# Kernel tuning notes

Measured on AMD Instinct MI355X. Metric: run time of the kernel, lower is better.

Reference implementation:

```python
import jax, jax.numpy as jnp
import numpy as np

N_BLOCKS = 16
BLOCK_SIZE = 512
TOP_K = N_BLOCKS // 4  # matches n_blocks // 4 in the source


def setup_inputs() -> dict:
    key = jax.random.key(0)
    k1, k2, k3, k4, k5 = jax.random.split(key, 5)
    in_f, out_f = 2048, 8192
    x = jax.random.normal(k1, (2, 4096, in_f), dtype=jnp.float32)
    # router: Linear(in_features, n_blocks)
    Wr = jax.random.normal(k2, (N_BLOCKS, in_f), dtype=jnp.float32) * (in_f ** -0.5)
    br = jnp.zeros((N_BLOCKS,), dtype=jnp.float32)
    # fc1: Linear(in, out); fc2: Linear(out, in). Biases are unused in the original forward.
    W1 = jax.random.normal(k3, (out_f, in_f), dtype=jnp.float32) * (in_f ** -0.5)
    W2 = jax.random.normal(k4, (in_f, out_f), dtype=jnp.float32) * (out_f ** -0.5)
    return {"x": x, "Wr": Wr, "br": br, "W1": W1, "W2": W2}


def reference(x, Wr, br, W1, W2):
    x_shape = x.shape
    in_f = x_shape[-1]
    xf = x.reshape(-1, in_f)                      # [N, in]
    n = xf.shape[0]
    # router + top-k block selection per token
    prob = jax.nn.softmax(xf @ Wr.T + br, axis=-1)          # [N, nb]
    _, idx = jax.lax.top_k(prob, TOP_K)                      # [N, k]
    mask = jnp.zeros((n, N_BLOCKS), dtype=xf.dtype)
    mask = mask.at[jnp.arange(n)[:, None], idx].set(1.0)     # [N, nb]
    # fc1 per block: h[n,i,b] = x @ W1_block_i^T  (bias never used in source)
    W1b = W1.reshape(N_BLOCKS, BLOCK_SIZE, in_f)
    h = jnp.einsum('nf,ibf->nib', xf, W1b)                   # [N, nb, bs]
    # activation, then zero out unselected blocks (unselected never reach fc2)
    h = jax.nn.gelu(h, approximate=False) * mask[:, :, None]
    # fc2 per block accumulate: y = sum_i h_i @ W2_block_i^T
    W2b = W2.reshape(in_f, N_BLOCKS, BLOCK_SIZE)
    y = jnp.einsum('nib,fib->nf', h, W2b)                    # [N, in]
    return y.reshape(x_shape)
```

## Files before the change

kernel.cpp:

```cpp
#include <hip/hip_runtime.h>
#include <hip/hip_bf16.h>

#define N_TOK 8192
#define IN_F  2048
#define OUT_F 8192
#define NB    16
#define BS    512
#define BM2   256
#define MAX_MT2 144

typedef short          bf16x8  __attribute__((ext_vector_type(8)));
typedef unsigned short ushort8 __attribute__((ext_vector_type(8)));
typedef float          f32x4   __attribute__((ext_vector_type(4)));
typedef _Float16       f16x8   __attribute__((ext_vector_type(8)));

#define WS_COUNTS 0
#define WS_TSTART 64
#define WS_SEL    256
#define WS_INV    (32*1024)
#define WS_LISTS  (192*1024)
#define WS_XBF    (1ull<<20)
#define WS_W2BF   WS_XBF
#define WS_H      (WS_XBF + 33554432ull)
#define WS_W1BF   (WS_H + 37748736ull)
#define WS_YP     WS_W1BF

static __device__ __forceinline__ unsigned short f2bf(float f) {
    __hip_bfloat16 h = __float2bfloat16(f);
    return *reinterpret_cast<unsigned short*>(&h);
}

static __device__ __forceinline__ void gload16(const unsigned short* g, unsigned short* lds) {
    __builtin_amdgcn_global_load_lds(
        (const __attribute__((address_space(1))) unsigned int*)g,
        (__attribute__((address_space(3))) unsigned int*)lds, 16, 0, 0);
}

#define MFMA16(ai, bi) \
    acc[0][0] = __builtin_amdgcn_mfma_f32_16x16x32_bf16(ai##0, bi##0, acc[0][0], 0, 0, 0); \
    acc[0][1] = __builtin_amdgcn_mfma_f32_16x16x32_bf16(ai##0, bi##1, acc[0][1], 0, 0, 0); \
    acc[0][2] = __builtin_amdgcn_mfma_f32_16x16x32_bf16(ai##0, bi##2, acc[0][2], 0, 0, 0); \
    acc[0][3] = __builtin_amdgcn_mfma_f32_16x16x32_bf16(ai##0, bi##3, acc[0][3], 0, 0, 0); \
    acc[1][0] = __builtin_amdgcn_mfma_f32_16x16x32_bf16(ai##1, bi##0, acc[1][0], 0, 0, 0); \
    acc[1][1] = __builtin_amdgcn_mfma_f32_16x16x32_bf16(ai##1, bi##1, acc[1][1], 0, 0, 0); \
    acc[1][2] = __builtin_amdgcn_mfma_f32_16x16x32_bf16(ai##1, bi##2, acc[1][2], 0, 0, 0); \
    acc[1][3] = __builtin_amdgcn_mfma_f32_16x16x32_bf16(ai##1, bi##3, acc[1][3], 0, 0, 0); \
    acc[2][0] = __builtin_amdgcn_mfma_f32_16x16x32_bf16(ai##2, bi##0, acc[2][0], 0, 0, 0); \
    acc[2][1] = __builtin_amdgcn_mfma_f32_16x16x32_bf16(ai##2, bi##1, acc[2][1], 0, 0, 0); \
    acc[2][2] = __builtin_amdgcn_mfma_f32_16x16x32_bf16(ai##2, bi##2, acc[2][2], 0, 0, 0); \
    acc[2][3] = __builtin_amdgcn_mfma_f32_16x16x32_bf16(ai##2, bi##3, acc[2][3], 0, 0, 0); \
    acc[3][0] = __builtin_amdgcn_mfma_f32_16x16x32_bf16(ai##3, bi##0, acc[3][0], 0, 0, 0); \
    acc[3][1] = __builtin_amdgcn_mfma_f32_16x16x32_bf16(ai##3, bi##1, acc[3][1], 0, 0, 0); \
    acc[3][2] = __builtin_amdgcn_mfma_f32_16x16x32_bf16(ai##3, bi##2, acc[3][2], 0, 0, 0); \
    acc[3][3] = __builtin_amdgcn_mfma_f32_16x16x32_bf16(ai##3, bi##3, acc[3][3], 0, 0, 0);

#define PHASE_TAIL \
    __builtin_amdgcn_s_barrier(); \
    asm volatile("s_waitcnt lgkmcnt(0)" ::: "memory"); \
    __builtin_amdgcn_sched_barrier(0); \
    __builtin_amdgcn_s_setprio(1); \
    MFMA16(a, b) \
    __builtin_amdgcn_s_setprio(0); \
    __builtin_amdgcn_sched_barrier(0); \
    __builtin_amdgcn_s_barrier();

__global__ __launch_bounds__(256) void router_kernel(
    const float* __restrict__ x, const float* __restrict__ Wr,
    const float* __restrict__ br, unsigned short* __restrict__ sel,
    unsigned short* __restrict__ x_bf)
{
    __shared__ float xs[4][IN_F];
    const int tid = threadIdx.x;
    const int lt = tid & 63;
    const int wv = tid >> 6;
    const int tok = blockIdx.x * 4 + wv;
    float4* xl = (float4*)xs[wv];
    const float4* xp = (const float4*)(x + (size_t)tok * IN_F);
    #pragma unroll
    for (int i = 0; i < 8; ++i) xl[lt + i * 64] = xp[lt + i * 64];
    __syncthreads();
    const int e = lt >> 2, p = lt & 3;
    const float4* wp = (const float4*)(Wr + (size_t)e * IN_F);
    double s = 0.0;
    for (int j = p; j < IN_F / 4; j += 4) {
        float4 a = xl[j], w = wp[j];
        s += (double)a.x * w.x + (double)a.y * w.y + (double)a.z * w.z + (double)a.w * w.w;
    }
    s += __shfl_down(s, 2);
    s += __shfl_down(s, 1);
    __shared__ double logits[4][NB];
    if (p == 0) logits[wv][e] = s + (double)br[e];
    __syncthreads();
    if (lt == 0) {
        unsigned used = 0, packed = 0;
        #pragma unroll
        for (int kk = 0; kk < 4; ++kk) {
            int best = 0; double bv = -1.0e300;
            #pragma unroll
            for (int i = 0; i < NB; ++i)
                if (!((used >> i) & 1u) && logits[wv][i] > bv) { bv = logits[wv][i]; best = i; }
            used |= 1u << best;
            packed |= (unsigned)best << (4 * kk);
        }
        sel[tok] = (unsigned short)packed;
    }
    const int t7 = tok & 7;
    unsigned short* drow = x_bf + (size_t)tok * IN_F;
    #pragma unroll
    for (int i = 0; i < 4; ++i) {
        const int slot = lt + i * 64;
        const float* sp = &xs[wv][slot * 8];
        ushort8 o;
        #pragma unroll
        for (int j = 0; j < 8; ++j) o[j] = f2bf(sp[j]);
        *(ushort8*)(drow + ((slot ^ t7) << 3)) = o;
    }
}

__global__ __launch_bounds__(256) void build_lists_kernel(
    const unsigned short* __restrict__ sel, int* __restrict__ counts,
    int* __restrict__ lists, unsigned* __restrict__ inv)
{
    const int e = blockIdx.x;
    const int t = threadIdx.x;
    unsigned short mysel[N_TOK / 256];
    int cnt = 0;
    #pragma unroll
    for (int i = 0; i < N_TOK / 256; ++i) {
        unsigned s = sel[i * 256 + t];
        mysel[i] = (unsigned short)s;
        bool m = ((s & 15u) == (unsigned)e) | (((s >> 4) & 15u) == (unsigned)e) |
                 (((s >> 8) & 15u) == (unsigned)e) | (((s >> 12) & 15u) == (unsigned)e);
        cnt += m ? 1 : 0;
    }
    __shared__ int ps[256];
    ps[t] = cnt;
    __syncthreads();
    #pragma unroll
    for (int off = 1; off < 256; off <<= 1) {
        int v = (t >= off) ? ps[t - off] : 0;
        __syncthreads();
        ps[t] += v;
        __syncthreads();
    }
    int pos = ps[t] - cnt;
    if (t == 255) counts[e] = ps[255];
    #pragma unroll
    for (int i = 0; i < N_TOK / 256; ++i) {
        unsigned s = mysel[i];
        bool m = ((s & 15u) == (unsigned)e) | (((s >> 4) & 15u) == (unsigned)e) |
                 (((s >> 8) & 15u) == (unsigned)e) | (((s >> 12) & 15u) == (unsigned)e);
        if (m) {
            const int tok = i * 256 + t;
            int j = ((s & 15u) == (unsigned)e) ? 0 :
                    (((s >> 4) & 15u) == (unsigned)e) ? 1 :
                    (((s >> 8) & 15u) == (unsigned)e) ? 2 : 3;
            inv[tok * 4 + j] = ((unsigned)e << 16) | (unsigned)pos;
            lists[e * N_TOK + pos++] = tok;
        }
    }
}

__global__ void scan_kernel(const int* __restrict__ counts, int* __restrict__ tstart)
{
    if (threadIdx.x == 0) {
        int acc = 0;
        for (int i = 0; i < NB; ++i) { tstart[i] = acc; acc += (counts[i] + BM2 - 1) / BM2; }
        tstart[NB] = acc;
    }
}

__global__ __launch_bounds__(256) void convert_swz_kernel(
    const float* __restrict__ src, unsigned short* __restrict__ dst, int sh)
{
    const int total = 1 << 21;
    for (int id = blockIdx.x * 256 + threadIdx.x; id < total; id += 2048 * 256) {
        const int row = id >> sh;
        const int sr  = id & ((1 << sh) - 1);
        const int ps  = sr ^ (row & 7);
        const float4* s4 = (const float4*)(src + ((size_t)id << 3));
        float4 p0 = s4[0], p1 = s4[1];
        ushort8 o;
        o[0] = f2bf(p0.x); o[1] = f2bf(p0.y); o[2] = f2bf(p0.z); o[3] = f2bf(p0.w);
        o[4] = f2bf(p1.x); o[5] = f2bf(p1.y); o[6] = f2bf(p1.z); o[7] = f2bf(p1.w);
        *(ushort8*)(dst + (((size_t)(row) << sh) << 3) + ((size_t)ps << 3)) = o;
    }
}

__global__ __launch_bounds__(512) void fc1_kernel(
    const unsigned short* __restrict__ x_bf, const unsigned short* __restrict__ w1_bf,
    const int* __restrict__ lists, const int* __restrict__ counts,
    const int* __restrict__ tstart, unsigned short* __restrict__ h)
{
    __shared__ unsigned short lds[73728];
    const int bid = blockIdx.x;
    const int newid = (bid & 7) * 72 + (bid >> 3);
    const int nt = newid & 3, mt = newid >> 2;
    if (mt >= tstart[NB]) return;
    int b = 0;
    #pragma unroll
    for (int i = 1; i < NB; ++i) b += (mt >= tstart[i]);
    const int cnt  = counts[b];
    const int row0 = (mt - tstart[b]) * BM2;
    const int tid  = threadIdx.x;
    const int wave = tid >> 6, lane = tid & 63;
    const int sph = lane & 7;
    const int rbase = wave * 8 + (lane >> 3);

    const unsigned short* aS[4];
    const unsigned short* bS[2];
    #pragma unroll
    for (int i = 0; i < 4; ++i) {
        const int r = i * 64 + rbase;
        const int gr = min(row0 + r, cnt - 1);
        const int tok = lists[b * N_TOK + gr];
        aS[i] = x_bf + (size_t)tok * IN_F + ((sph ^ (r & 7) ^ (tok & 7)) << 3);
    }
    #pragma unroll
    for (int j = 0; j < 2; ++j) {
        const int r = j * 64 + rbase;
        bS[j] = w1_bf + (size_t)(b * BS + nt * 128 + r) * IN_F + (sph << 3);
    }
    const int wbase = wave * 512;

    const int lr16 = lane & 15, q = lane >> 4;
    const int wm = (wave >> 1) * 64, wn = (wave & 1) * 64;
    int offA[4], offB[4];
    #pragma unroll
    for (int i = 0; i < 4; ++i) { const int r = wm + i * 16 + lr16; offA[i] = r * 64 + ((q ^ (r & 7)) << 3); }
    #pragma unroll
    for (int j = 0; j < 4; ++j) { const int r = wn + j * 16 + lr16; offB[j] = r * 64 + ((q ^ (r & 7)) << 3); }

    f32x4 acc[4][4];
    #pragma unroll
    for (int i = 0; i < 4; ++i)
        #pragma unroll
        for (int j = 0; j < 4; ++j) acc[i][j] = (f32x4)0.0f;

#define STA1(k, buf, i) gload16(aS[i] + (size_t)(k) * 64, lds + (buf) * 24576 + (i) * 4096 + wbase)
#define STB1(k, buf, j) gload16(bS[j] + (size_t)(k) * 64, lds + (buf) * 24576 + 16384 + (j) * 4096 + wbase)

    STA1(0,0,0); STA1(0,0,1); STA1(0,0,2); STA1(0,0,3); STB1(0,0,0); STB1(0,0,1);
    STA1(1,1,0); STA1(1,1,1); STA1(1,1,2); STA1(1,1,3); STB1(1,1,0); STB1(1,1,1);
    asm volatile("s_waitcnt vmcnt(6)" ::: "memory");
    __builtin_amdgcn_s_barrier();

    const int NK = IN_F / 64;
    int cur = 0;
    for (int k = 0; k < NK; ++k) {
        const unsigned short* Ab = lds + cur * 24576;
        const unsigned short* Bb = Ab + 16384;
        const int nxt = (cur == 0) ? 2 : cur - 1;
        bf16x8 a0 = *(const bf16x8*)&Ab[offA[0]];
        bf16x8 a1 = *(const bf16x8*)&Ab[offA[1]];
        bf16x8 a2 = *(const bf16x8*)&Ab[offA[2]];
        bf16x8 a3 = *(const bf16x8*)&Ab[offA[3]];
        bf16x8 b0 = *(const bf16x8*)&Bb[offB[0]];
        bf16x8 b1 = *(const bf16x8*)&Bb[offB[1]];
        bf16x8 b2 = *(const bf16x8*)&Bb[offB[2]];
        bf16x8 b3 = *(const bf16x8*)&Bb[offB[3]];
        if (k + 2 < NK) { STA1(k + 2, nxt, 0); STA1(k + 2, nxt, 1); STB1(k + 2, nxt, 0); }
        PHASE_TAIL
        a0 = *(const bf16x8*)&Ab[offA[0] ^ 32];
        a1 = *(const bf16x8*)&Ab[offA[1] ^ 32];
        a2 = *(const bf16x8*)&Ab[offA[2] ^ 32];
        a3 = *(const bf16x8*)&Ab[offA[3] ^ 32];
        b0 = *(const bf16x8*)&Bb[offB[0] ^ 32];
        b1 = *(const bf16x8*)&Bb[offB[1] ^ 32];
        b2 = *(const bf16x8*)&Bb[offB[2] ^ 32];
        b3 = *(const bf16x8*)&Bb[offB[3] ^ 32];
        if (k + 2 < NK) {
            STA1(k + 2, nxt, 2); STA1(k + 2, nxt, 3); STB1(k + 2, nxt, 1);
            asm volatile("s_waitcnt vmcnt(6)" ::: "memory");
        } else if (k + 1 < NK) {
            asm volatile("s_waitcnt vmcnt(0)" ::: "memory");
        }
        PHASE_TAIL
        cur = (cur == 2) ? 0 : cur + 1;
    }
    #pragma unroll
    for (int i = 0; i < 4; ++i) {
        #pragma unroll
        for (int r = 0; r < 4; ++r) {
            const int lrow = wm + i * 16 + q * 4 + r;
            if (row0 + lrow < cnt) {
                const size_t hrow = (size_t)(mt * BM2 + lrow) * BS;
                const int r7 = (lrow & 7) << 3;
                #pragma unroll
                for (int j = 0; j < 4; ++j) {
                    const int col = nt * 128 + wn + j * 16 + lr16;
                    float v = acc[i][j][r];
                    v = 0.5f * v * (1.0f + erff(v * 0.70710678118654752f));
                    h[hrow + (col ^ r7)] = f2bf(v);
                }
            }
        }
    }
#undef STA1
#undef STB1
}

__global__ __launch_bounds__(512) void fc2_kernel(
    const unsigned short* __restrict__ h, const unsigned short* __restrict__ w2_bf,
    const int* __restrict__ counts, const int* __restrict__ tstart,
    _Float16* __restrict__ yp)
{
    __shared__ unsigned short lds[2][32768];
    const int bid = blockIdx.x;
    const int newid = (bid & 7) * 144 + (bid >> 3);
    const int nt = newid & 7, mt = newid >> 3;
    if (mt >= tstart[NB]) return;
    int b = 0;
    #pragma unroll
    for (int i = 1; i < NB; ++i) b += (mt >= tstart[i]);
    const int cnt  = counts[b];
    const int row0 = (mt - tstart[b]) * BM2;
    const int tid  = threadIdx.x;
    const int wave = tid >> 6, lane = tid & 63;
    const int sph = lane & 7;
    const int rbase = wave * 8 + (lane >> 3);

    const unsigned short* aS[4];
    const unsigned short* bS[4];
    #pragma unroll
    for (int g = 0; g < 4; ++g) {
        const int r = g * 64 + rbase;
        aS[g] = h + (size_t)(mt * BM2 + r) * BS + (sph << 3);
        bS[g] = w2_bf + (size_t)(nt * 256 + r) * OUT_F + b * BS + (sph << 3);
    }
    const int wbase = wave * 512;

    const int lr16 = lane & 15, q = lane >> 4;
    const int wr = (wave >> 2) * 128, wc = (wave & 3) * 64;
    int offA[8], offB[4];
    #pragma unroll
    for (int i = 0; i < 8; ++i) { const int r = wr + i * 16 + lr16; offA[i] = r * 64 + ((q ^ (r & 7)) << 3); }
    #pragma unroll
    for (int j = 0; j < 4; ++j) { const int r = wc + j * 16 + lr16; offB[j] = 16384 + r * 64 + ((q ^ (r & 7)) << 3); }

    f32x4 acc[8][4];
    #pragma unroll
    for (int i = 0; i < 8; ++i)
        #pragma unroll
        for (int j = 0; j < 4; ++j) acc[i][j] = (f32x4)0.0f;

#define ST2(k, buf) \
    { _Pragma("unroll") for (int g = 0; g < 4; ++g) \
        gload16(aS[g] + (size_t)(k) * 64, &lds[buf][g * 4096 + wbase]); \
      _Pragma("unroll") for (int g = 0; g < 4; ++g) \
        gload16(bS[g] + (size_t)(k) * 64, &lds[buf][16384 + g * 4096 + wbase]); }

#define MFMA_8x4 \
    __builtin_amdgcn_s_barrier(); \
    asm volatile("s_waitcnt lgkmcnt(0)" ::: "memory"); \
    __builtin_amdgcn_sched_barrier(0); \
    __builtin_amdgcn_s_setprio(1); \
    _Pragma("unroll") for (int i = 0; i < 8; ++i) \
        _Pragma("unroll") for (int j = 0; j < 4; ++j) \
            acc[i][j] = __builtin_amdgcn_mfma_f32_16x16x32_bf16(a[i], bb[j], acc[i][j], 0, 0, 0); \
    __builtin_amdgcn_s_setprio(0); \
    __builtin_amdgcn_sched_barrier(0); \
    __builtin_amdgcn_s_barrier();

    ST2(0, 0);
    asm volatile("s_waitcnt vmcnt(0)" ::: "memory");
    __builtin_amdgcn_s_barrier();

    const int NK = BS / 64;
    for (int k = 0; k < NK; ++k) {
        const int cur = k & 1;
        const unsigned short* L = lds[cur];
        {
            bf16x8 a[8], bb[4];
            #pragma unroll
            for (int i = 0; i < 8; ++i) a[i]  = *(const bf16x8*)&L[offA[i]];
            #pragma unroll
            for (int j = 0; j < 4; ++j) bb[j] = *(const bf16x8*)&L[offB[j]];
            if (k + 1 < NK) ST2(k + 1, cur ^ 1);
            MFMA_8x4
        }
        {
            bf16x8 a[8], bb[4];
            #pragma unroll
            for (int i = 0; i < 8; ++i) a[i]  = *(const bf16x8*)&L[offA[i] ^ 32];
            #pragma unroll
            for (int j = 0; j < 4; ++j) bb[j] = *(const bf16x8*)&L[offB[j] ^ 32];
            if (k + 1 < NK) asm volatile("s_waitcnt vmcnt(0)" ::: "memory");
            MFMA_8x4
        }
    }
    #pragma unroll
    for (int i = 0; i < 8; ++i) {
        #pragma unroll
        for (int r = 0; r < 4; ++r) {
            const int lrow = wr + i * 16 + q * 4 + r;
            if (row0 + lrow < cnt) {
                _Float16* yrow = yp + (size_t)(mt * BM2 + lrow) * IN_F + nt * 256 + wc + lr16;
                #pragma unroll
                for (int j = 0; j < 4; ++j)
                    yrow[j * 16] = (_Float16)acc[i][j][r];
            }
        }
    }
#undef ST2
#undef MFMA_8x4
}

__global__ __launch_bounds__(256) void reduce_kernel(
    const _Float16* __restrict__ yp, const unsigned* __restrict__ inv,
    const int* __restrict__ tstart, float* __restrict__ y)
{
    const int tok = blockIdx.x;
    __shared__ size_t rbase[4];
    if (threadIdx.x < 4) {
        unsigned v = inv[tok * 4 + threadIdx.x];
        rbase[threadIdx.x] = (size_t)(tstart[v >> 16] * BM2 + (int)(v & 0xFFFFu)) * IN_F;
    }
    __syncthreads();
    const int c = threadIdx.x * 8;
    f16x8 v0 = *(const f16x8*)(yp + rbase[0] + c);
    f16x8 v1 = *(const f16x8*)(yp + rbase[1] + c);
    f16x8 v2 = *(const f16x8*)(yp + rbase[2] + c);
    f16x8 v3 = *(const f16x8*)(yp + rbase[3] + c);
    float out[8];
    #pragma unroll
    for (int j = 0; j < 8; ++j)
        out[j] = (float)v0[j] + (float)v1[j] + (float)v2[j] + (float)v3[j];
    float4* yo = (float4*)(y + (size_t)tok * IN_F + c);
    yo[0] = make_float4(out[0], out[1], out[2], out[3]);
    yo[1] = make_float4(out[4], out[5], out[6], out[7]);
}

extern "C" void kernel_launch(void* const* d_in, const int* in_sizes, int n_in,
                              void* d_out, int out_size, void* d_ws, size_t ws_size,
                              hipStream_t stream) {
    const float* x  = (const float*)d_in[0];
    const float* Wr = (const float*)d_in[1];
    const float* br = (const float*)d_in[2];
    const float* W1 = (const float*)d_in[3];
    const float* W2 = (const float*)d_in[4];
    float* y = (float*)d_out;
    char* ws = (char*)d_ws;
    int* counts = (int*)(ws + WS_COUNTS);
    int* tstart = (int*)(ws + WS_TSTART);
    unsigned short* sel = (unsigned short*)(ws + WS_SEL);
    unsigned* inv = (unsigned*)(ws + WS_INV);
    int* lists  = (int*)(ws + WS_LISTS);
    unsigned short* x_bf  = (unsigned short*)(ws + WS_XBF);
    unsigned short* w1_bf = (unsigned short*)(ws + WS_W1BF);
    unsigned short* w2_bf = (unsigned short*)(ws + WS_W2BF);
    unsigned short* h     = (unsigned short*)(ws + WS_H);
    _Float16* yp          = (_Float16*)(ws + WS_YP);

    hipLaunchKernelGGL(router_kernel, dim3(N_TOK / 4), dim3(256), 0, stream, x, Wr, br, sel, x_bf);
    hipLaunchKernelGGL(build_lists_kernel, dim3(NB), dim3(256), 0, stream, sel, counts, lists, inv);
    hipLaunchKernelGGL(scan_kernel, dim3(1), dim3(64), 0, stream, counts, tstart);
    hipLaunchKernelGGL(convert_swz_kernel, dim3(2048), dim3(256), 0, stream, W1, w1_bf, 8);
    hipLaunchKernelGGL(fc1_kernel, dim3(4 * MAX_MT2), dim3(512), 0, stream, x_bf, w1_bf, lists, counts, tstart, h);
    hipLaunchKernelGGL(convert_swz_kernel, dim3(2048), dim3(256), 0, stream, W2, w2_bf, 10);
    hipLaunchKernelGGL(fc2_kernel, dim3(8 * MAX_MT2), dim3(512), 0, stream, h, w2_bf, counts, tstart, yp);
    hipLaunchKernelGGL(reduce_kernel, dim3(N_TOK), dim3(256), 0, stream, yp, inv, tstart, y);
}
```

Baseline: 397.5 us.

## Enlarge fc1 tile to 256x256 with double-buffered pipeline shared with fc2

The fc1 kernel moves from a 256x128 output tile with a triple-buffered, split-phase load schedule to a 256x256 tile per block. Each wave now holds an 8x4 MFMA accumulator grid, and the kernel reuses the double-buffered load and MFMA macro that fc2 already uses. This halves the fc1 grid and raises operand reuse per LDS byte, cutting global and LDS traffic per FLOP. The cost is more accumulator registers, lower occupancy, fewer blocks to balance across CUs, and a full vmcnt(0) wait each k-step instead of partial overlap.

```diff
diff --git a/kernel.cpp b/kernel.cpp
--- a/kernel.cpp
+++ b/kernel.cpp
@@ -36,30 +36,14 @@
         (__attribute__((address_space(3))) unsigned int*)lds, 16, 0, 0);
 }
 
-#define MFMA16(ai, bi) \
-    acc[0][0] = __builtin_amdgcn_mfma_f32_16x16x32_bf16(ai##0, bi##0, acc[0][0], 0, 0, 0); \
-    acc[0][1] = __builtin_amdgcn_mfma_f32_16x16x32_bf16(ai##0, bi##1, acc[0][1], 0, 0, 0); \
-    acc[0][2] = __builtin_amdgcn_mfma_f32_16x16x32_bf16(ai##0, bi##2, acc[0][2], 0, 0, 0); \
-    acc[0][3] = __builtin_amdgcn_mfma_f32_16x16x32_bf16(ai##0, bi##3, acc[0][3], 0, 0, 0); \
-    acc[1][0] = __builtin_amdgcn_mfma_f32_16x16x32_bf16(ai##1, bi##0, acc[1][0], 0, 0, 0); \
-    acc[1][1] = __builtin_amdgcn_mfma_f32_16x16x32_bf16(ai##1, bi##1, acc[1][1], 0, 0, 0); \
-    acc[1][2] = __builtin_amdgcn_mfma_f32_16x16x32_bf16(ai##1, bi##2, acc[1][2], 0, 0, 0); \
-    acc[1][3] = __builtin_amdgcn_mfma_f32_16x16x32_bf16(ai##1, bi##3, acc[1][3], 0, 0, 0); \
-    acc[2][0] = __builtin_amdgcn_mfma_f32_16x16x32_bf16(ai##2, bi##0, acc[2][0], 0, 0, 0); \
-    acc[2][1] = __builtin_amdgcn_mfma_f32_16x16x32_bf16(ai##2, bi##1, acc[2][1], 0, 0, 0); \
-    acc[2][2] = __builtin_amdgcn_mfma_f32_16x16x32_bf16(ai##2, bi##2, acc[2][2], 0, 0, 0); \
-    acc[2][3] = __builtin_amdgcn_mfma_f32_16x16x32_bf16(ai##2, bi##3, acc[2][3], 0, 0, 0); \
-    acc[3][0] = __builtin_amdgcn_mfma_f32_16x16x32_bf16(ai##3, bi##0, acc[3][0], 0, 0, 0); \
-    acc[3][1] = __builtin_amdgcn_mfma_f32_16x16x32_bf16(ai##3, bi##1, acc[3][1], 0, 0, 0); \
-    acc[3][2] = __builtin_amdgcn_mfma_f32_16x16x32_bf16(ai##3, bi##2, acc[3][2], 0, 0, 0); \
-    acc[3][3] = __builtin_amdgcn_mfma_f32_16x16x32_bf16(ai##3, bi##3, acc[3][3], 0, 0, 0);
-
-#define PHASE_TAIL \
+#define MFMA_8x4 \
     __builtin_amdgcn_s_barrier(); \
     asm volatile("s_waitcnt lgkmcnt(0)" ::: "memory"); \
     __builtin_amdgcn_sched_barrier(0); \
     __builtin_amdgcn_s_setprio(1); \
-    MFMA16(a, b) \
+    _Pragma("unroll") for (int i = 0; i < 8; ++i) \
+        _Pragma("unroll") for (int j = 0; j < 4; ++j) \
+            acc[i][j] = __builtin_amdgcn_mfma_f32_16x16x32_bf16(a[i], bb[j], acc[i][j], 0, 0, 0); \
     __builtin_amdgcn_s_setprio(0); \
     __builtin_amdgcn_sched_barrier(0); \
     __builtin_amdgcn_s_barrier();
@@ -192,10 +176,10 @@
     const int* __restrict__ lists, const int* __restrict__ counts,
     const int* __restrict__ tstart, unsigned short* __restrict__ h)
 {
-    __shared__ unsigned short lds[73728];
+    __shared__ unsigned short lds[2][32768];
     const int bid = blockIdx.x;
-    const int newid = (bid & 7) * 72 + (bid >> 3);
-    const int nt = newid & 3, mt = newid >> 2;
+    const int newid = (bid & 7) * 36 + (bid >> 3);
+    const int nt = newid & 1, mt = newid >> 1;
     if (mt >= tstart[NB]) return;
     int b = 0;
     #pragma unroll
@@ -208,87 +192,75 @@
     const int rbase = wave * 8 + (lane >> 3);
 
     const unsigned short* aS[4];
-    const unsigned short* bS[2];
-    #pragma unroll
-    for (int i = 0; i < 4; ++i) {
-        const int r = i * 64 + rbase;
+    const unsigned short* bS[4];
+    #pragma unroll
+    for (int g = 0; g < 4; ++g) {
+        const int r = g * 64 + rbase;
         const int gr = min(row0 + r, cnt - 1);
         const int tok = lists[b * N_TOK + gr];
-        aS[i] = x_bf + (size_t)tok * IN_F + ((sph ^ (r & 7) ^ (tok & 7)) << 3);
-    }
-    #pragma unroll
-    for (int j = 0; j < 2; ++j) {
-        const int r = j * 64 + rbase;
-        bS[j] = w1_bf + (size_t)(b * BS + nt * 128 + r) * IN_F + (sph << 3);
+        aS[g] = x_bf + (size_t)tok * IN_F + ((sph ^ (r & 7) ^ (tok & 7)) << 3);
+        bS[g] = w1_bf + (size_t)(b * BS + nt * 256 + r) * IN_F + (sph << 3);
     }
     const int wbase = wave * 512;
 
     const int lr16 = lane & 15, q = lane >> 4;
-    const int wm = (wave >> 1) * 64, wn = (wave & 1) * 64;
-    int offA[4], offB[4];
-    #pragma unroll
-    for (int i = 0; i < 4; ++i) { const int r = wm + i * 16 + lr16; offA[i] = r * 64 + ((q ^ (r & 7)) << 3); }
-    #pragma unroll
-    for (int j = 0; j < 4; ++j) { const int r = wn + j * 16 + lr16; offB[j] = r * 64 + ((q ^ (r & 7)) << 3); }
-
-    f32x4 acc[4][4];
-    #pragma unroll
-    for (int i = 0; i < 4; ++i)
+    const int wr = (wave >> 2) * 128, wc = (wave & 3) * 64;
+    int offA[8], offB[4];
+    #pragma unroll
+    for (int i = 0; i < 8; ++i) { const int r = wr + i * 16 + lr16; offA[i] = r * 64 + ((q ^ (r & 7)) << 3); }
+    #pragma unroll
+    for (int j = 0; j < 4; ++j) { const int r = wc + j * 16 + lr16; offB[j] = 16384 + r * 64 + ((q ^ (r & 7)) << 3); }
+
+    f32x4 acc[8][4];
+    #pragma unroll
+    for (int i = 0; i < 8; ++i)
         #pragma unroll
         for (int j = 0; j < 4; ++j) acc[i][j] = (f32x4)0.0f;
 
-#define STA1(k, buf, i) gload16(aS[i] + (size_t)(k) * 64, lds + (buf) * 24576 + (i) * 4096 + wbase)
-#define STB1(k, buf, j) gload16(bS[j] + (size_t)(k) * 64, lds + (buf) * 24576 + 16384 + (j) * 4096 + wbase)
-
-    STA1(0,0,0); STA1(0,0,1); STA1(0,0,2); STA1(0,0,3); STB1(0,0,0); STB1(0,0,1);
-    STA1(1,1,0); STA1(1,1,1); STA1(1,1,2); STA1(1,1,3); STB1(1,1,0); STB1(1,1,1);
-    asm volatile("s_waitcnt vmcnt(6)" ::: "memory");
+#define ST1(k, buf) \
+    { _Pragma("unroll") for (int g = 0; g < 4; ++g) \
+        gload16(aS[g] + (size_t)(k) * 64, &lds[buf][g * 4096 + wbase]); \
+      _Pragma("unroll") for (int g = 0; g < 4; ++g) \
+        gload16(bS[g] + (size_t)(k) * 64, &lds[buf][16384 + g * 4096 + wbase]); }
+
+    ST1(0, 0);
+    asm volatile("s_waitcnt vmcnt(0)" ::: "memory");
     __builtin_amdgcn_s_barrier();
 
     const int NK = IN_F / 64;
-    int cur = 0;
     for (int k = 0; k < NK; ++k) {
-        const unsigned short* Ab = lds + cur * 24576;
-        const unsigned short* Bb = Ab + 16384;
-        const int nxt = (cur == 0) ? 2 : cur - 1;
-        bf16x8 a0 = *(const bf16x8*)&Ab[offA[0]];
-        bf16x8 a1 = *(const bf16x8*)&Ab[offA[1]];
-        bf16x8 a2 = *(const bf16x8*)&Ab[offA[2]];
-        bf16x8 a3 = *(const bf16x8*)&Ab[offA[3]];
-        bf16x8 b0 = *(const bf16x8*)&Bb[offB[0]];
-        bf16x8 b1 = *(const bf16x8*)&Bb[offB[1]];
-        bf16x8 b2 = *(const bf16x8*)&Bb[offB[2]];
-        bf16x8 b3 = *(const bf16x8*)&Bb[offB[3]];
-        if (k + 2 < NK) { STA1(k + 2, nxt, 0); STA1(k + 2, nxt, 1); STB1(k + 2, nxt, 0); }
-        PHASE_TAIL
-        a0 = *(const bf16x8*)&Ab[offA[0] ^ 32];
-        a1 = *(const bf16x8*)&Ab[offA[1] ^ 32];
-        a2 = *(const bf16x8*)&Ab[offA[2] ^ 32];
-        a3 = *(const bf16x8*)&Ab[offA[3] ^ 32];
-        b0 = *(const bf16x8*)&Bb[offB[0] ^ 32];
-        b1 = *(const bf16x8*)&Bb[offB[1] ^ 32];
-        b2 = *(const bf16x8*)&Bb[offB[2] ^ 32];
-        b3 = *(const bf16x8*)&Bb[offB[3] ^ 32];
-        if (k + 2 < NK) {
-            STA1(k + 2, nxt, 2); STA1(k + 2, nxt, 3); STB1(k + 2, nxt, 1);
-            asm volatile("s_waitcnt vmcnt(6)" ::: "memory");
-        } else if (k + 1 < NK) {
-            asm volatile("s_waitcnt vmcnt(0)" ::: "memory");
-        }
-        PHASE_TAIL
-        cur = (cur == 2) ? 0 : cur + 1;
-    }
-    #pragma unroll
-    for (int i = 0; i < 4; ++i) {
+        const int cur = k & 1;
+        const unsigned short* L = lds[cur];
+        {
+            bf16x8 a[8], bb[4];
+            #pragma unroll
+            for (int i = 0; i < 8; ++i) a[i]  = *(const bf16x8*)&L[offA[i]];
+            #pragma unroll
+            for (int j = 0; j < 4; ++j) bb[j] = *(const bf16x8*)&L[offB[j]];
+            if (k + 1 < NK) ST1(k + 1, cur ^ 1);
+            MFMA_8x4
+        }
+        {
+            bf16x8 a[8], bb[4];
+            #pragma unroll
+            for (int i = 0; i < 8; ++i) a[i]  = *(const bf16x8*)&L[offA[i] ^ 32];
+            #pragma unroll
+            for (int j = 0; j < 4; ++j) bb[j] = *(const bf16x8*)&L[offB[j] ^ 32];
+            if (k + 1 < NK) asm volatile("s_waitcnt vmcnt(0)" ::: "memory");
+            MFMA_8x4
+        }
+    }
+    #pragma unroll
+    for (int i = 0; i < 8; ++i) {
         #pragma unroll
         for (int r = 0; r < 4; ++r) {
-            const int lrow = wm + i * 16 + q * 4 + r;
+            const int lrow = wr + i * 16 + q * 4 + r;
             if (row0 + lrow < cnt) {
                 const size_t hrow = (size_t)(mt * BM2 + lrow) * BS;
                 const int r7 = (lrow & 7) << 3;
                 #pragma unroll
                 for (int j = 0; j < 4; ++j) {
-                    const int col = nt * 128 + wn + j * 16 + lr16;
+                    const int col = nt * 256 + wc + j * 16 + lr16;
                     float v = acc[i][j][r];
                     v = 0.5f * v * (1.0f + erff(v * 0.70710678118654752f));
                     h[hrow + (col ^ r7)] = f2bf(v);
@@ -296,8 +268,7 @@
             }
         }
     }
-#undef STA1
-#undef STB1
+#undef ST1
 }
 
 __global__ __launch_bounds__(512) void fc2_kernel(
@@ -349,18 +320,6 @@
         gload16(aS[g] + (size_t)(k) * 64, &lds[buf][g * 4096 + wbase]); \
       _Pragma("unroll") for (int g = 0; g < 4; ++g) \
         gload16(bS[g] + (size_t)(k) * 64, &lds[buf][16384 + g * 4096 + wbase]); }
-
-#define MFMA_8x4 \
-    __builtin_amdgcn_s_barrier(); \
-    asm volatile("s_waitcnt lgkmcnt(0)" ::: "memory"); \
-    __builtin_amdgcn_sched_barrier(0); \
-    __builtin_amdgcn_s_setprio(1); \
-    _Pragma("unroll") for (int i = 0; i < 8; ++i) \
-        _Pragma("unroll") for (int j = 0; j < 4; ++j) \
-            acc[i][j] = __builtin_amdgcn_mfma_f32_16x16x32_bf16(a[i], bb[j], acc[i][j], 0, 0, 0); \
-    __builtin_amdgcn_s_setprio(0); \
-    __builtin_amdgcn_sched_barrier(0); \
-    __builtin_amdgcn_s_barrier();
 
     ST2(0, 0);
     asm volatile("s_waitcnt vmcnt(0)" ::: "memory");
@@ -403,7 +362,6 @@
         }
     }
 #undef ST2
-#undef MFMA_8x4
 }
 
 __global__ __launch_bounds__(256) void reduce_kernel(
@@ -456,7 +414,7 @@
     hipLaunchKernelGGL(build_lists_kernel, dim3(NB), dim3(256), 0, stream, sel, counts, lists, inv);
     hipLaunchKernelGGL(scan_kernel, dim3(1), dim3(64), 0, stream, counts, tstart);
     hipLaunchKernelGGL(convert_swz_kernel, dim3(2048), dim3(256), 0, stream, W1, w1_bf, 8);
-    hipLaunchKernelGGL(fc1_kernel, dim3(4 * MAX_MT2), dim3(512), 0, stream, x_bf, w1_bf, lists, counts, tstart, h);
+    hipLaunchKernelGGL(fc1_kernel, dim3(2 * MAX_MT2), dim3(512), 0, stream, x_bf, w1_bf, lists, counts, tstart, h);
     hipLaunchKernelGGL(convert_swz_kernel, dim3(2048), dim3(256), 0, stream, W2, w2_bf, 10);
     hipLaunchKernelGGL(fc2_kernel, dim3(8 * MAX_MT2), dim3(512), 0, stream, h, w2_bf, counts, tstart, yp);
     hipLaunchKernelGGL(reduce_kernel, dim3(N_TOK), dim3(256), 0, stream, yp, inv, tstart, y);
```

Measured after the change: 472.6 us. +18.9%, slower.
